# Performance work log

Measured on AMD Instinct MI355X. Metric: run time of the kernel, lower is better.

## Reference

```python
import jax, jax.numpy as jnp
import numpy as np

EPS = 1e-5
GROUPS = 32


def conv2d(x, w, b):
    # x: [N,C,H,W], w: [O,I,3,3] (or 1x1), stride 1, padding 'same' for 3x3
    kh = w.shape[2]
    pad = (kh - 1) // 2
    y = jax.lax.conv_general_dilated(x, w, (1, 1), ((pad, pad), (pad, pad)),
                                     dimension_numbers=('NCHW', 'OIHW', 'NCHW'))
    return y + b[None, :, None, None]


def group_norm(x, g, b):
    N, C, H, W = x.shape
    xr = x.reshape(N, GROUPS, C // GROUPS, H, W)
    mu = xr.mean(axis=(2, 3, 4), keepdims=True)
    var = xr.var(axis=(2, 3, 4), keepdims=True)
    xr = (xr - mu) / jnp.sqrt(var + EPS)
    return xr.reshape(N, C, H, W) * g[None, :, None, None] + b[None, :, None, None]


def batch_norm(x, g, b):
    # training-mode BatchNorm2d: batch statistics over (N,H,W)
    mu = x.mean(axis=(0, 2, 3), keepdims=True)
    var = x.var(axis=(0, 2, 3), keepdims=True)
    return (x - mu) / jnp.sqrt(var + EPS) * g[None, :, None, None] + b[None, :, None, None]


def binary_activation(x):
    # STE: forward sign(x), backward through piecewise poly out3
    out_fwd = jnp.sign(x)
    m1 = (x < -1).astype(x.dtype)
    m2 = (x < 0).astype(x.dtype)
    m3 = (x < 1).astype(x.dtype)
    out1 = -1.0 * m1 + (x * x + 2.0 * x) * (1.0 - m1)
    out2 = out1 * m2 + (-x * x + 2.0 * x) * (1.0 - m2)
    out3 = out2 * m3 + 1.0 * (1.0 - m3)
    return jax.lax.stop_gradient(out_fwd - out3) + out3


def hard_binary_conv(x, w, b):
    # per-output-channel scaling * sign(w), STE through clipped weights
    scale = jax.lax.stop_gradient(jnp.mean(jnp.abs(w), axis=(1, 2, 3), keepdims=True))
    bw_ng = scale * jnp.sign(w)
    clipped = jnp.clip(w, -1.0, 1.0)
    bw = jax.lax.stop_gradient(bw_ng - clipped) + clipped
    return conv2d(x, bw, b)


def learnable_bias(x, emb, w, b):
    bias = jax.nn.silu(emb) @ w.T + b  # [B, C]
    return x + bias[:, :, None, None]


def _forward(c, x, emb,
             rb_gn1_g, rb_gn1_b, rb_conv1_w, rb_conv1_b, rb_emb_w, rb_emb_b,
             rb_gn2_g, rb_gn2_b, rb_conv2_w, rb_conv2_b,
             m1_w, m1_b, bconv_w, bconv_b, bn_g, bn_b,
             m2_w, m2_b, prelu_a, m3_w, m3_b):
    # ResBlock (skip = Identity since out_channels == channels)
    h = conv2d(jax.nn.silu(group_norm(c, rb_gn1_g, rb_gn1_b)), rb_conv1_w, rb_conv1_b)
    eo = jax.nn.silu(emb) @ rb_emb_w.T + rb_emb_b          # [B, 2*C]
    scale, shift = jnp.split(eo[:, :, None, None], 2, axis=1)
    h = group_norm(h, rb_gn2_g, rb_gn2_b) * (1.0 + scale) + shift
    h = conv2d(jax.nn.silu(h), rb_conv2_w, rb_conv2_b)
    c2 = c + h
    # concat + bias + STE binarize + binary conv + BN + channel-pool residual + PReLU
    xc = jnp.concatenate([x, c2], axis=1)                   # [B, 2C, H, W]
    out = learnable_bias(xc, emb, m1_w, m1_b)
    out = binary_activation(out)
    out = hard_binary_conv(out, bconv_w, bconv_b)
    out = batch_norm(out, bn_g, bn_b)
    N, C2, H, W = xc.shape
    out = out + xc.reshape(N, C2 // 2, 2, H, W).mean(axis=2)  # channel mean pooling
    out = learnable_bias(out, emb, m2_w, m2_b)
    out = jnp.where(out >= 0, out, prelu_a[None, :, None, None] * out)  # PReLU
    out = learnable_bias(out, emb, m3_w, m3_b)
    return out


def setup_inputs() -> dict:
    key = jax.random.key(0)
    ks = jax.random.split(key, 24)
    B, C, EMB, H, W = 8, 128, 512, 64, 64
    IN2 = 2 * C
    n = lambda k, s, sc=0.05: jax.random.normal(k, s, dtype=jnp.float32) * sc
    return {
        'c': jax.random.normal(ks[0], (B, C, H, W), dtype=jnp.float32),
        'x': jax.random.normal(ks[1], (B, C, H, W), dtype=jnp.float32),
        'emb': jax.random.normal(ks[2], (B, EMB), dtype=jnp.float32),
        'rb_gn1_g': jnp.ones((C,), jnp.float32), 'rb_gn1_b': jnp.zeros((C,), jnp.float32),
        'rb_conv1_w': n(ks[3], (C, C, 3, 3)), 'rb_conv1_b': n(ks[4], (C,)),
        'rb_emb_w': n(ks[5], (2 * C, EMB)), 'rb_emb_b': n(ks[6], (2 * C,)),
        'rb_gn2_g': jnp.ones((C,), jnp.float32), 'rb_gn2_b': jnp.zeros((C,), jnp.float32),
        'rb_conv2_w': n(ks[7], (C, C, 3, 3)), 'rb_conv2_b': n(ks[8], (C,)),
        'm1_w': n(ks[9], (IN2, EMB)), 'm1_b': n(ks[10], (IN2,)),
        'bconv_w': jax.random.uniform(ks[11], (C, IN2, 3, 3), dtype=jnp.float32) * 0.001,
        'bconv_b': n(ks[12], (C,)),
        'bn_g': jnp.ones((C,), jnp.float32), 'bn_b': jnp.zeros((C,), jnp.float32),
        'm2_w': n(ks[13], (C, EMB)), 'm2_b': n(ks[14], (C,)),
        'prelu_a': jnp.full((C,), 0.25, jnp.float32),
        'm3_w': n(ks[15], (C, EMB)), 'm3_b': n(ks[16], (C,)),
    }


def reference(c, x, emb,
              rb_gn1_g, rb_gn1_b, rb_conv1_w, rb_conv1_b, rb_emb_w, rb_emb_b,
              rb_gn2_g, rb_gn2_b, rb_conv2_w, rb_conv2_b,
              m1_w, m1_b, bconv_w, bconv_b, bn_g, bn_b,
              m2_w, m2_b, prelu_a, m3_w, m3_b):
    return _forward(c, x, emb,
                    rb_gn1_g, rb_gn1_b, rb_conv1_w, rb_conv1_b, rb_emb_w, rb_emb_b,
                    rb_gn2_g, rb_gn2_b, rb_conv2_w, rb_conv2_b,
                    m1_w, m1_b, bconv_w, bconv_b, bn_g, bn_b,
                    m2_w, m2_b, prelu_a, m3_w, m3_b)
```

## Files before the change

kernel.cpp:

```cpp
#include <hip/hip_runtime.h>
#include <stdint.h>


#define B_   8
#define C_   128
#define C2_  256
#define HW_  4096
#define EMB_ 512
#define EPS_ 1e-5f

typedef int   v16i __attribute__((ext_vector_type(16)));
typedef float v16f __attribute__((ext_vector_type(16)));
typedef short v8s  __attribute__((ext_vector_type(8)));
typedef int   v4i  __attribute__((ext_vector_type(4)));

#define COLB 272
#define LDSZ (3 * 66 * COLB)

__device__ __forceinline__ float silu(float v) { return v / (1.f + expf(-v)); }
__device__ __forceinline__ unsigned short f2bf(float f) {
    unsigned int x = __float_as_uint(f);
    return (unsigned short)((x + 0x7FFFu + ((x >> 16) & 1u)) >> 16);
}
__device__ __forceinline__ int8_t sgn8(float v) {
    return (v > 0.f) ? (int8_t)1 : ((v < 0.f) ? (int8_t)(-1) : (int8_t)0);
}

__global__ __launch_bounds__(256) void k_prep(
    const float* __restrict__ w, int8_t* __restrict__ sgn,
    float* __restrict__ alpha, float* __restrict__ bnS, float* __restrict__ bnQ,
    float* __restrict__ gnS, float* __restrict__ gnQ,
    const float* __restrict__ w1, const float* __restrict__ w2,
    unsigned short* __restrict__ Wc1, unsigned short* __restrict__ Wc2,
    const float* __restrict__ emb,
    const float* __restrict__ ew, const float* __restrict__ ebb,
    const float* __restrict__ m1w, const float* __restrict__ m1b,
    const float* __restrict__ m2w, const float* __restrict__ m2b,
    const float* __restrict__ m3w, const float* __restrict__ m3b,
    float* __restrict__ eo, float* __restrict__ b1,
    float* __restrict__ b2, float* __restrict__ b3) {
    __shared__ float red[256];
    const int blk = blockIdx.x, tid = threadIdx.x;
    if (blk < 128) {
        const int o = blk;
        if (o == 0 && tid < 128) { bnS[tid] = 0.f; bnQ[tid] = 0.f; }
        if (o == 1) { gnS[tid] = 0.f; }
        if (o == 2) { gnQ[tid] = 0.f; }
        const float* wr = w + (size_t)o * (C2_ * 9);
        float s = 0.f;
        for (int i = tid; i < C2_ * 9; i += 256) s += fabsf(wr[i]);
        red[tid] = s;
        __syncthreads();
        for (int st = 128; st > 0; st >>= 1) {
            if (tid < st) red[tid] += red[tid + st];
            __syncthreads();
        }
        if (tid == 0) alpha[o] = red[0] / (float)(C2_ * 9);
        for (int kk = 0; kk < 9; ++kk) {
            float v = wr[tid * 9 + kk];
            sgn[((size_t)(kk * 16 + (tid >> 4)) * C_ + o) * 16 + (tid & 15)] = sgn8(v);
        }
    } else if (blk < 704) {
        int i = (blk - 128) * 256 + tid;
        int co = i / (C_ * 9);
        int rem = i - co * (C_ * 9);
        int ci = rem / 9, kk = rem - ci * 9;
        size_t d = ((size_t)(kk * 16 + (ci >> 3)) * C_ + co) * 8 + (ci & 7);
        Wc1[d] = f2bf(w1[i]);
        Wc2[d] = f2bf(w2[i]);
    } else {
        const int o = (blk - 704) * 4 + (tid >> 6);
        const int l = tid & 63;
        const float* wv;
        float bias;
        float* dst;
        int dstride;
        if (o < 256)      { wv = ew  + (size_t)o * EMB_;              bias = ebb[o];    dst = eo + o;  dstride = 256; }
        else if (o < 512) { int r = o - 256; wv = m1w + (size_t)r * EMB_; bias = m1b[r]; dst = b1 + r; dstride = 256; }
        else if (o < 640) { int r = o - 512; wv = m2w + (size_t)r * EMB_; bias = m2b[r]; dst = b2 + r; dstride = 128; }
        else              { int r = o - 640; wv = m3w + (size_t)r * EMB_; bias = m3b[r]; dst = b3 + r; dstride = 128; }
        const float4 wa = *(const float4*)(wv + 8 * l);
        const float4 wb = *(const float4*)(wv + 8 * l + 4);
#pragma unroll
        for (int b = 0; b < B_; ++b) {
            const float* s = emb + b * EMB_ + 8 * l;
            float4 sa = *(const float4*)(s);
            float4 sb = *(const float4*)(s + 4);
            float p = wa.x * silu(sa.x) + wa.y * silu(sa.y) + wa.z * silu(sa.z) + wa.w * silu(sa.w) +
                      wb.x * silu(sb.x) + wb.y * silu(sb.y) + wb.z * silu(sb.z) + wb.w * silu(sb.w);
#pragma unroll
            for (int off = 32; off > 0; off >>= 1) p += __shfl_down(p, off, 64);
            if (l == 0) dst[b * dstride] = bias + p;
        }
    }
}

__global__ __launch_bounds__(1024) void k_gn1t(const float* __restrict__ in,
                                               const float* __restrict__ g,
                                               const float* __restrict__ b,
                                               unsigned short* __restrict__ act) {
    __shared__ float ssum[1024], ssq[1024];
    __shared__ float s_mu, s_rstd;
    const int tid = threadIdx.x;
    const int n = blockIdx.x >> 5, grp = blockIdx.x & 31;
    const size_t base = ((size_t)(n * C_ + grp * 4)) << 12;
    float sum = 0.f, sq = 0.f;
    const float4* in4 = (const float4*)(in + base);
    for (int i = tid; i < 4096; i += 1024) {
        float4 v = in4[i];
        sum += v.x + v.y + v.z + v.w;
        sq += v.x * v.x + v.y * v.y + v.z * v.z + v.w * v.w;
    }
    ssum[tid] = sum; ssq[tid] = sq;
    __syncthreads();
    for (int st = 512; st > 0; st >>= 1) {
        if (tid < st) { ssum[tid] += ssum[tid + st]; ssq[tid] += ssq[tid + st]; }
        __syncthreads();
    }
    if (tid == 0) {
        float mu = ssum[0] * (1.f / 16384.f);
        float var = ssq[0] * (1.f / 16384.f) - mu * mu;
        s_mu = mu; s_rstd = rsqrtf(var + EPS_);
    }
    __syncthreads();
    const float mu = s_mu, rstd = s_rstd;
    float gg[4], bb[4];
#pragma unroll
    for (int j = 0; j < 4; ++j) { gg[j] = g[grp * 4 + j]; bb[j] = b[grp * 4 + j]; }
    for (int hw = tid; hw < HW_; hw += 1024) {
        union { unsigned short u[4]; uint2 v; } pk;
#pragma unroll
        for (int j = 0; j < 4; ++j) {
            float v = in[base + ((size_t)j << 12) + hw];
            pk.u[j] = f2bf(silu((v - mu) * rstd * gg[j] + bb[j]));
        }
        *(uint2*)(act + ((size_t)(n * HW_ + hw)) * C_ + grp * 4) = pk.v;
    }
}

__global__ __launch_bounds__(1024) void k_gn2a(const float* __restrict__ in,
                                               const float* __restrict__ g,
                                               const float* __restrict__ b,
                                               const float* __restrict__ eo,
                                               const float* __restrict__ gnS,
                                               const float* __restrict__ gnQ,
                                               unsigned short* __restrict__ act) {
    const int tid = threadIdx.x;
    const int n = blockIdx.x >> 5, grp = blockIdx.x & 31;
    const size_t base = ((size_t)(n * C_ + grp * 4)) << 12;
    const float mu = gnS[n * 32 + grp] * (1.f / 16384.f);
    const float var = gnQ[n * 32 + grp] * (1.f / 16384.f) - mu * mu;
    const float rstd = rsqrtf(var + EPS_);
    float sc[4], sh[4], gg[4], bb[4];
#pragma unroll
    for (int j = 0; j < 4; ++j) {
        int ch = grp * 4 + j;
        gg[j] = g[ch]; bb[j] = b[ch];
        sc[j] = 1.f + eo[n * 256 + ch];
        sh[j] = eo[n * 256 + 128 + ch];
    }
    for (int hw = tid; hw < HW_; hw += 1024) {
        union { unsigned short u[4]; uint2 v; } pk;
#pragma unroll
        for (int j = 0; j < 4; ++j) {
            float v = in[base + ((size_t)j << 12) + hw];
            float y = ((v - mu) * rstd * gg[j] + bb[j]) * sc[j] + sh[j];
            pk.u[j] = f2bf(silu(y));
        }
        *(uint2*)(act + ((size_t)(n * HW_ + hw)) * C_ + grp * 4) = pk.v;
    }
}

__device__ __forceinline__ void stage_rows(char* lds, const char* rs0,
                                           const char* rs1, const char* rs2) {
    const int tid = threadIdx.x;
    const char* rs[3] = {rs0, rs1, rs2};
    if (tid < 96) {
        int r = tid / 32, q = tid & 31;
        int c = (q >> 4) ? 65 : 0, o = q & 15;
        *(float4*)(lds + (r * 66 + c) * COLB + o * 16) = make_float4(0.f, 0.f, 0.f, 0.f);
    }
#pragma unroll
    for (int u = 0; u < 12; ++u) {
        int idx = u * 256 + tid;
        int r = idx >> 10, rem = idx & 1023;
        int x = rem >> 4, o = rem & 15;
        char* dst = lds + (r * 66 + x + 1) * COLB + o * 16;
        if (rs[r]) *(float4*)dst = *(const float4*)(rs[r] + x * 256 + o * 16);
        else       *(float4*)dst = make_float4(0.f, 0.f, 0.f, 0.f);
    }
}

__global__ __launch_bounds__(256) void k_conv1(const unsigned short* __restrict__ act,
                                               const unsigned short* __restrict__ Wc,
                                               const float* __restrict__ bias,
                                               float* __restrict__ out,
                                               float* __restrict__ gnS,
                                               float* __restrict__ gnQ) {
    __shared__ __align__(16) char lds[LDSZ];
    const int y = blockIdx.x;
    const int n = blockIdx.y;
    const char* base = (const char*)(act + ((size_t)n * 64) * 64 * C_);
    stage_rows(lds,
               (y > 0)  ? base + (size_t)(y - 1) * 16384 : nullptr,
               base + (size_t)y * 16384,
               (y < 63) ? base + (size_t)(y + 1) * 16384 : nullptr);
    __syncthreads();

    const int w = threadIdx.x >> 6;
    const int l = threadIdx.x & 63;
    const int lm = l & 31;
    const int lh = l >> 5;

    v16f acc0, acc1;
#pragma unroll
    for (int i = 0; i < 16; ++i) { acc0[i] = 0.f; acc1[i] = 0.f; }

#pragma unroll
    for (int kk = 0; kk < 9; ++kk) {
        const int r = kk / 3, dx = kk % 3 - 1;
        const char* col0 = lds + (r * 66 + lm + 1 + dx) * COLB + 16 * lh;
        const char* col1 = col0 + 32 * COLB;
        const unsigned short* wbase = Wc + (size_t)(kk * 16 + lh) * C_ * 8 + (32 * w + lm) * 8;
#pragma unroll
        for (int cb = 0; cb < 8; ++cb) {
            v8s a = *(const v8s*)(wbase + (size_t)(2 * cb) * C_ * 8);
            v8s b0 = *(const v8s*)(col0 + 32 * cb);
            v8s b1 = *(const v8s*)(col1 + 32 * cb);
            acc0 = __builtin_amdgcn_mfma_f32_32x32x16_bf16(a, b0, acc0, 0, 0, 0);
            acc1 = __builtin_amdgcn_mfma_f32_32x32x16_bf16(a, b1, acc1, 0, 0, 0);
        }
    }
    float pr[16], qr[16];
#pragma unroll
    for (int r = 0; r < 16; ++r) {
        const int row = (r & 3) + 8 * (r >> 2) + 4 * lh;
        const int co = 32 * w + row;
        const float bv = bias[co];
        const size_t o = (((size_t)n * C_ + co) << 12) + (y << 6);
        float v0 = acc0[r] + bv, v1 = acc1[r] + bv;
        out[o + lm] = v0;
        out[o + 32 + lm] = v1;
        pr[r] = v0 + v1;
        qr[r] = v0 * v0 + v1 * v1;
    }
    __syncthreads();
    float* ldsS = (float*)lds;
    float* ldsQ = (float*)lds + 128;
#pragma unroll
    for (int r = 0; r < 16; ++r) {
        float p = pr[r], q = qr[r];
#pragma unroll
        for (int m = 16; m > 0; m >>= 1) {
            p += __shfl_xor(p, m, 64);
            q += __shfl_xor(q, m, 64);
        }
        if (lm == 0) {
            const int row = (r & 3) + 8 * (r >> 2) + 4 * lh;
            const int co = 32 * w + row;
            ldsS[co] = p;
            ldsQ[co] = q;
        }
    }
    __syncthreads();
    if (threadIdx.x < 32) {
        const int g = threadIdx.x;
        float p = ldsS[4 * g] + ldsS[4 * g + 1] + ldsS[4 * g + 2] + ldsS[4 * g + 3];
        float q = ldsQ[4 * g] + ldsQ[4 * g + 1] + ldsQ[4 * g + 2] + ldsQ[4 * g + 3];
        atomicAdd(&gnS[n * 32 + g], p);
        atomicAdd(&gnQ[n * 32 + g], q);
    }
}

__global__ __launch_bounds__(256) void k_conv2(const unsigned short* __restrict__ act,
                                               const unsigned short* __restrict__ Wc,
                                               const float* __restrict__ bias,
                                               const float* __restrict__ res,
                                               const float* __restrict__ xin,
                                               const float* __restrict__ b1v,
                                               float* __restrict__ out,
                                               int8_t* __restrict__ S) {
    __shared__ __align__(16) char lds[LDSZ];
    const int y = blockIdx.x;
    const int n = blockIdx.y;
    const char* base = (const char*)(act + ((size_t)n * 64) * 64 * C_);
    stage_rows(lds,
               (y > 0)  ? base + (size_t)(y - 1) * 16384 : nullptr,
               base + (size_t)y * 16384,
               (y < 63) ? base + (size_t)(y + 1) * 16384 : nullptr);
    __syncthreads();

    const int w = threadIdx.x >> 6;
    const int l = threadIdx.x & 63;
    const int lm = l & 31;
    const int lh = l >> 5;

    v16f acc0, acc1;
#pragma unroll
    for (int i = 0; i < 16; ++i) { acc0[i] = 0.f; acc1[i] = 0.f; }

#pragma unroll
    for (int kk = 0; kk < 9; ++kk) {
        const int r = kk / 3, dx = kk % 3 - 1;
        const char* col0 = lds + (r * 66 + lm + 1 + dx) * COLB + 16 * lh;
        const char* col1 = col0 + 32 * COLB;
        const unsigned short* wbase = Wc + (size_t)(kk * 16 + lh) * C_ * 8 + (32 * w + lm) * 8;
#pragma unroll
        for (int cb = 0; cb < 8; ++cb) {
            v8s a = *(const v8s*)(wbase + (size_t)(2 * cb) * C_ * 8);
            v8s b0 = *(const v8s*)(col0 + 32 * cb);
            v8s b1 = *(const v8s*)(col1 + 32 * cb);
            acc0 = __builtin_amdgcn_mfma_f32_32x32x16_bf16(a, b0, acc0, 0, 0, 0);
            acc1 = __builtin_amdgcn_mfma_f32_32x32x16_bf16(a, b1, acc1, 0, 0, 0);
        }
    }
    float c2v0[16], c2v1[16];
#pragma unroll
    for (int r = 0; r < 16; ++r) {
        const int row = (r & 3) + 8 * (r >> 2) + 4 * lh;
        const int co = 32 * w + row;
        const float bv = bias[co];
        const size_t o = (((size_t)n * C_ + co) << 12) + (y << 6);
        float v0 = acc0[r] + bv + res[o + lm];
        float v1 = acc1[r] + bv + res[o + 32 + lm];
        out[o + lm] = v0;
        out[o + 32 + lm] = v1;
        c2v0[r] = v0;
        c2v1[r] = v1;
    }

    __syncthreads();
#pragma unroll
    for (int q = 0; q < 4; ++q) {
        const int co0 = 32 * w + 8 * q + 4 * lh;
        const float b0 = b1v[n * 256 + 128 + co0];
        const float b1b = b1v[n * 256 + 128 + co0 + 1];
        const float b2b = b1v[n * 256 + 128 + co0 + 2];
        const float b3b = b1v[n * 256 + 128 + co0 + 3];
        union { int8_t b[4]; int u; } p0, p1;
        p0.b[0] = sgn8(c2v0[4 * q] + b0);  p1.b[0] = sgn8(c2v1[4 * q] + b0);
        p0.b[1] = sgn8(c2v0[4 * q + 1] + b1b); p1.b[1] = sgn8(c2v1[4 * q + 1] + b1b);
        p0.b[2] = sgn8(c2v0[4 * q + 2] + b2b); p1.b[2] = sgn8(c2v1[4 * q + 2] + b2b);
        p0.b[3] = sgn8(c2v0[4 * q + 3] + b3b); p1.b[3] = sgn8(c2v1[4 * q + 3] + b3b);
        *(int*)(lds + lm * COLB + 128 + co0) = p0.u;
        *(int*)(lds + (32 + lm) * COLB + 128 + co0) = p1.u;
    }
#pragma unroll
    for (int u = 0; u < 8; ++u) {
        int idx = u * 256 + threadIdx.x;
        int ch = idx >> 4, seg = idx & 15;
        float4 v = *(const float4*)(xin + (((size_t)(n * C_ + ch)) << 12) + (y << 6) + 4 * seg);
        const float bv = b1v[n * 256 + ch];
        lds[(4 * seg) * COLB + ch]     = sgn8(v.x + bv);
        lds[(4 * seg + 1) * COLB + ch] = sgn8(v.y + bv);
        lds[(4 * seg + 2) * COLB + ch] = sgn8(v.z + bv);
        lds[(4 * seg + 3) * COLB + ch] = sgn8(v.w + bv);
    }
    __syncthreads();
    int8_t* Srow = S + ((size_t)(n * HW_) + (y << 6)) * C2_;
#pragma unroll
    for (int u = 0; u < 4; ++u) {
        int idx = u * 256 + threadIdx.x;
        int px = idx >> 4, c16 = idx & 15;
        *(int4*)(Srow + (size_t)px * C2_ + 16 * c16) = *(const int4*)(lds + px * COLB + 16 * c16);
    }
}

__global__ __launch_bounds__(256) void k_bconv(const int8_t* __restrict__ S,
                                               const int8_t* __restrict__ Wk,
                                               const float* __restrict__ alpha,
                                               const float* __restrict__ bias,
                                               float* __restrict__ out,
                                               float* __restrict__ bnS,
                                               float* __restrict__ bnQ) {
    __shared__ __align__(16) char lds[LDSZ];
    const int y = blockIdx.x;
    const int n = blockIdx.y;
    const char* base = (const char*)(S + ((size_t)n * 64) * 64 * C2_);
    stage_rows(lds,
               (y > 0)  ? base + (size_t)(y - 1) * 16384 : nullptr,
               base + (size_t)y * 16384,
               (y < 63) ? base + (size_t)(y + 1) * 16384 : nullptr);
    __syncthreads();

    const int w = threadIdx.x >> 6;
    const int l = threadIdx.x & 63;
    const int lm = l & 31;
    const int lh = l >> 5;

    v16i acc0, acc1;
#pragma unroll
    for (int i = 0; i < 16; ++i) { acc0[i] = 0; acc1[i] = 0; }

#pragma unroll
    for (int kk = 0; kk < 9; ++kk) {
        const int r = kk / 3, dx = kk % 3 - 1;
        const char* col0 = lds + (r * 66 + lm + 1 + dx) * COLB + 16 * lh;
        const char* col1 = col0 + 32 * COLB;
        const int8_t* wbase = Wk + (size_t)(kk * 16 + lh) * C_ * 16 + (32 * w + lm) * 16;
#pragma unroll
        for (int s = 0; s < 8; ++s) {
            v4i a = *(const v4i*)(wbase + (size_t)(2 * s) * C_ * 16);
            v4i b0 = *(const v4i*)(col0 + 32 * s);
            v4i b1 = *(const v4i*)(col1 + 32 * s);
            acc0 = __builtin_amdgcn_mfma_i32_32x32x32_i8(a, b0, acc0, 0, 0, 0);
            acc1 = __builtin_amdgcn_mfma_i32_32x32x32_i8(a, b1, acc1, 0, 0, 0);
        }
    }

    float pr[16], qr[16];
#pragma unroll
    for (int r = 0; r < 16; ++r) {
        const int row = (r & 3) + 8 * (r >> 2) + 4 * lh;
        const int co = 32 * w + row;
        const float av = alpha[co], bv = bias[co];
        const size_t o = (((size_t)n * C_ + co) << 12) + (y << 6);
        float v0 = av * (float)acc0[r] + bv;
        float v1 = av * (float)acc1[r] + bv;
        out[o + lm]      = v0;
        out[o + 32 + lm] = v1;
        pr[r] = v0 + v1;
        qr[r] = v0 * v0 + v1 * v1;
    }
    __syncthreads();
    float* ldsS = (float*)lds;
    float* ldsQ = (float*)lds + 128;
#pragma unroll
    for (int r = 0; r < 16; ++r) {
        float p = pr[r], q = qr[r];
#pragma unroll
        for (int m = 16; m > 0; m >>= 1) {
            p += __shfl_xor(p, m, 64);
            q += __shfl_xor(q, m, 64);
        }
        if (lm == 0) {
            const int row = (r & 3) + 8 * (r >> 2) + 4 * lh;
            const int co = 32 * w + row;
            ldsS[co] = p;
            ldsQ[co] = q;
        }
    }
    __syncthreads();
    if (threadIdx.x < 128) {
        atomicAdd(&bnS[threadIdx.x], ldsS[threadIdx.x]);
        atomicAdd(&bnQ[threadIdx.x], ldsQ[threadIdx.x]);
    }
}

__global__ __launch_bounds__(256) void k_final(const float* __restrict__ y3,
                                               const float* __restrict__ x,
                                               const float* __restrict__ c2,
                                               const float* __restrict__ bnS,
                                               const float* __restrict__ bnQ,
                                               const float* __restrict__ bng,
                                               const float* __restrict__ bnb,
                                               const float* __restrict__ b2v,
                                               const float* __restrict__ pa,
                                               const float* __restrict__ b3v,
                                               float* __restrict__ out) {
    const int idx4 = blockIdx.x * 256 + threadIdx.x;
    const int hw = (idx4 & 1023) * 4;
    const int cb = idx4 >> 10;
    const int co = cb & 127;
    const int n = cb >> 7;
    const float mu = bnS[co] * (1.f / 32768.f);
    const float var = bnQ[co] * (1.f / 32768.f) - mu * mu;
    const float rstd = rsqrtf(var + EPS_);
    const float gm = rstd * bng[co];
    const float bt = bnb[co] - mu * gm;
    const size_t obase = (((size_t)(n * C_ + co)) << 12) + hw;
    float4 v = *(const float4*)(y3 + obase);
    v.x = v.x * gm + bt; v.y = v.y * gm + bt; v.z = v.z * gm + bt; v.w = v.w * gm + bt;

    const int ch0 = 2 * co;
    float4 pA, pB;
    if (co < 64) {
        pA = *(const float4*)(x + (((size_t)(n * C_ + ch0)) << 12) + hw);
        pB = *(const float4*)(x + (((size_t)(n * C_ + ch0 + 1)) << 12) + hw);
    } else {
        int d = ch0 - 128;
        pA = *(const float4*)(c2 + (((size_t)(n * C_ + d)) << 12) + hw);
        pB = *(const float4*)(c2 + (((size_t)(n * C_ + d + 1)) << 12) + hw);
    }
    const float bias2 = b2v[n * 128 + co];
    const float aP = pa[co];
    const float bias3 = b3v[n * 128 + co];
    float4 r;
    float t;
    t = v.x + 0.5f * (pA.x + pB.x) + bias2; t = (t >= 0.f) ? t : aP * t; r.x = t + bias3;
    t = v.y + 0.5f * (pA.y + pB.y) + bias2; t = (t >= 0.f) ? t : aP * t; r.y = t + bias3;
    t = v.z + 0.5f * (pA.z + pB.z) + bias2; t = (t >= 0.f) ? t : aP * t; r.z = t + bias3;
    t = v.w + 0.5f * (pA.w + pB.w) + bias2; t = (t >= 0.f) ? t : aP * t; r.w = t + bias3;
    *(float4*)(out + obase) = r;
}

extern "C" void kernel_launch(void* const* d_in, const int* in_sizes, int n_in,
                              void* d_out, int out_size, void* d_ws, size_t ws_size,
                              hipStream_t stream) {
    const float* c       = (const float*)d_in[0];
    const float* x       = (const float*)d_in[1];
    const float* emb     = (const float*)d_in[2];
    const float* gn1_g   = (const float*)d_in[3];
    const float* gn1_b   = (const float*)d_in[4];
    const float* conv1_w = (const float*)d_in[5];
    const float* conv1_b = (const float*)d_in[6];
    const float* emb_w   = (const float*)d_in[7];
    const float* emb_b   = (const float*)d_in[8];
    const float* gn2_g   = (const float*)d_in[9];
    const float* gn2_b   = (const float*)d_in[10];
    const float* conv2_w = (const float*)d_in[11];
    const float* conv2_b = (const float*)d_in[12];
    const float* m1_w    = (const float*)d_in[13];
    const float* m1_b    = (const float*)d_in[14];
    const float* bconv_w = (const float*)d_in[15];
    const float* bconv_b = (const float*)d_in[16];
    const float* bn_g    = (const float*)d_in[17];
    const float* bn_b    = (const float*)d_in[18];
    const float* m2_w    = (const float*)d_in[19];
    const float* m2_b    = (const float*)d_in[20];
    const float* prelu_a = (const float*)d_in[21];
    const float* m3_w    = (const float*)d_in[22];
    const float* m3_b    = (const float*)d_in[23];
    float* out = (float*)d_out;

    float* ws = (float*)d_ws;
    const size_t NCHW = (size_t)B_ * C_ * HW_;
    float*  a_buf = ws;
    float*  y_buf = ws + NCHW;
    unsigned short* actA = (unsigned short*)(ws + 2 * NCHW);
    int8_t* S     = (int8_t*)(ws + 2 * NCHW);
    int8_t* sgn   = (int8_t*)(ws + 2 * NCHW + NCHW / 2);
    unsigned short* Wc1 = (unsigned short*)(ws + 2 * NCHW + NCHW / 2 + 73728);
    unsigned short* Wc2 = Wc1 + C_ * C_ * 9;
    float*  alpha = ws + 2 * NCHW + NCHW / 2 + 73728 + 2 * 73728;
    float*  eo    = alpha + 128;
    float*  b1v   = eo + B_ * 256;
    float*  b2v   = b1v + B_ * 256;
    float*  b3v   = b2v + B_ * 128;
    float*  bnS   = b3v + B_ * 128;
    float*  bnQ   = bnS + 128;
    float*  gnS   = bnQ + 128;
    float*  gnQ   = gnS + 256;

    k_prep<<<896, 256, 0, stream>>>(bconv_w, sgn, alpha, bnS, bnQ, gnS, gnQ,
                                    conv1_w, conv2_w, Wc1, Wc2,
                                    emb, emb_w, emb_b, m1_w, m1_b, m2_w, m2_b,
                                    m3_w, m3_b, eo, b1v, b2v, b3v);
    k_gn1t<<<B_ * 32, 1024, 0, stream>>>(c, gn1_g, gn1_b, actA);
    k_conv1<<<dim3(64, B_), 256, 0, stream>>>(actA, Wc1, conv1_b, y_buf, gnS, gnQ);
    k_gn2a<<<B_ * 32, 1024, 0, stream>>>(y_buf, gn2_g, gn2_b, eo, gnS, gnQ, actA);
    k_conv2<<<dim3(64, B_), 256, 0, stream>>>(actA, Wc2, conv2_b, c, x, b1v, a_buf, S);
    k_bconv<<<dim3(64, B_), 256, 0, stream>>>(S, sgn, alpha, bconv_b, y_buf, bnS, bnQ);
    k_final<<<NCHW / 1024, 256, 0, stream>>>(y_buf, x, a_buf, bnS, bnQ, bn_g, bn_b,
                                             b2v, prelu_a, b3v, out);
}
```

Before: 255.4 us.

## Fuse GN1 into prep kernel and GN2 normalization into conv2 staging

The GroupNorm1+SiLU kernel is folded into the prep kernel as extra blocks, which removes one launch and lets it run alongside the weight preparation. The GroupNorm2+modulation+SiLU pass is moved into conv2's LDS staging: conv2 now reads fp32 y1 rows directly, normalizes and converts them to bf16 in shared memory, and no longer needs the intermediate activation buffer. In exchange, each conv2 block recomputes the normalized values for three input rows (a halo redundancy of about 3x). Staging now uses only 192 threads with strided per-channel stores, which may be slower than the previous cooperative copy.

```diff
diff --git a/kernel.cpp b/kernel.cpp
--- a/kernel.cpp
+++ b/kernel.cpp
@@ -38,8 +38,12 @@
     const float* __restrict__ m2w, const float* __restrict__ m2b,
     const float* __restrict__ m3w, const float* __restrict__ m3b,
     float* __restrict__ eo, float* __restrict__ b1,
-    float* __restrict__ b2, float* __restrict__ b3) {
-    __shared__ float red[256];
+    float* __restrict__ b2, float* __restrict__ b3,
+    const float* __restrict__ cin,
+    const float* __restrict__ g1, const float* __restrict__ bb1,
+    unsigned short* __restrict__ act) {
+    __shared__ float red[256], red2[256];
+    __shared__ float s_mu, s_rstd;
     const int blk = blockIdx.x, tid = threadIdx.x;
     if (blk < 128) {
         const int o = blk;
@@ -68,7 +72,7 @@
         size_t d = ((size_t)(kk * 16 + (ci >> 3)) * C_ + co) * 8 + (ci & 7);
         Wc1[d] = f2bf(w1[i]);
         Wc2[d] = f2bf(w2[i]);
-    } else {
+    } else if (blk < 896) {
         const int o = (blk - 704) * 4 + (tid >> 6);
         const int l = tid & 63;
         const float* wv;
@@ -92,82 +96,42 @@
             for (int off = 32; off > 0; off >>= 1) p += __shfl_down(p, off, 64);
             if (l == 0) dst[b * dstride] = bias + p;
         }
-    }
-}
-
-__global__ __launch_bounds__(1024) void k_gn1t(const float* __restrict__ in,
-                                               const float* __restrict__ g,
-                                               const float* __restrict__ b,
-                                               unsigned short* __restrict__ act) {
-    __shared__ float ssum[1024], ssq[1024];
-    __shared__ float s_mu, s_rstd;
-    const int tid = threadIdx.x;
-    const int n = blockIdx.x >> 5, grp = blockIdx.x & 31;
-    const size_t base = ((size_t)(n * C_ + grp * 4)) << 12;
-    float sum = 0.f, sq = 0.f;
-    const float4* in4 = (const float4*)(in + base);
-    for (int i = tid; i < 4096; i += 1024) {
-        float4 v = in4[i];
-        sum += v.x + v.y + v.z + v.w;
-        sq += v.x * v.x + v.y * v.y + v.z * v.z + v.w * v.w;
-    }
-    ssum[tid] = sum; ssq[tid] = sq;
-    __syncthreads();
-    for (int st = 512; st > 0; st >>= 1) {
-        if (tid < st) { ssum[tid] += ssum[tid + st]; ssq[tid] += ssq[tid + st]; }
+    } else {
+        const int bid = blk - 896;
+        const int n = bid >> 5, grp = bid & 31;
+        const size_t base = ((size_t)(n * C_ + grp * 4)) << 12;
+        float sum = 0.f, sq = 0.f;
+        const float4* in4 = (const float4*)(cin + base);
+        for (int i = tid; i < 4096; i += 256) {
+            float4 v = in4[i];
+            sum += v.x + v.y + v.z + v.w;
+            sq += v.x * v.x + v.y * v.y + v.z * v.z + v.w * v.w;
+        }
+        red[tid] = sum; red2[tid] = sq;
         __syncthreads();
-    }
-    if (tid == 0) {
-        float mu = ssum[0] * (1.f / 16384.f);
-        float var = ssq[0] * (1.f / 16384.f) - mu * mu;
-        s_mu = mu; s_rstd = rsqrtf(var + EPS_);
-    }
-    __syncthreads();
-    const float mu = s_mu, rstd = s_rstd;
-    float gg[4], bb[4];
-#pragma unroll
-    for (int j = 0; j < 4; ++j) { gg[j] = g[grp * 4 + j]; bb[j] = b[grp * 4 + j]; }
-    for (int hw = tid; hw < HW_; hw += 1024) {
-        union { unsigned short u[4]; uint2 v; } pk;
-#pragma unroll
-        for (int j = 0; j < 4; ++j) {
-            float v = in[base + ((size_t)j << 12) + hw];
-            pk.u[j] = f2bf(silu((v - mu) * rstd * gg[j] + bb[j]));
-        }
-        *(uint2*)(act + ((size_t)(n * HW_ + hw)) * C_ + grp * 4) = pk.v;
-    }
-}
-
-__global__ __launch_bounds__(1024) void k_gn2a(const float* __restrict__ in,
-                                               const float* __restrict__ g,
-                                               const float* __restrict__ b,
-                                               const float* __restrict__ eo,
-                                               const float* __restrict__ gnS,
-                                               const float* __restrict__ gnQ,
-                                               unsigned short* __restrict__ act) {
-    const int tid = threadIdx.x;
-    const int n = blockIdx.x >> 5, grp = blockIdx.x & 31;
-    const size_t base = ((size_t)(n * C_ + grp * 4)) << 12;
-    const float mu = gnS[n * 32 + grp] * (1.f / 16384.f);
-    const float var = gnQ[n * 32 + grp] * (1.f / 16384.f) - mu * mu;
-    const float rstd = rsqrtf(var + EPS_);
-    float sc[4], sh[4], gg[4], bb[4];
-#pragma unroll
-    for (int j = 0; j < 4; ++j) {
-        int ch = grp * 4 + j;
-        gg[j] = g[ch]; bb[j] = b[ch];
-        sc[j] = 1.f + eo[n * 256 + ch];
-        sh[j] = eo[n * 256 + 128 + ch];
-    }
-    for (int hw = tid; hw < HW_; hw += 1024) {
-        union { unsigned short u[4]; uint2 v; } pk;
-#pragma unroll
-        for (int j = 0; j < 4; ++j) {
-            float v = in[base + ((size_t)j << 12) + hw];
-            float y = ((v - mu) * rstd * gg[j] + bb[j]) * sc[j] + sh[j];
-            pk.u[j] = f2bf(silu(y));
-        }
-        *(uint2*)(act + ((size_t)(n * HW_ + hw)) * C_ + grp * 4) = pk.v;
+        for (int st = 128; st > 0; st >>= 1) {
+            if (tid < st) { red[tid] += red[tid + st]; red2[tid] += red2[tid + st]; }
+            __syncthreads();
+        }
+        if (tid == 0) {
+            float mu = red[0] * (1.f / 16384.f);
+            float var = red2[0] * (1.f / 16384.f) - mu * mu;
+            s_mu = mu; s_rstd = rsqrtf(var + EPS_);
+        }
+        __syncthreads();
+        const float mu = s_mu, rstd = s_rstd;
+        float gg[4], bbv[4];
+#pragma unroll
+        for (int j = 0; j < 4; ++j) { gg[j] = g1[grp * 4 + j]; bbv[j] = bb1[grp * 4 + j]; }
+        for (int hw = tid; hw < HW_; hw += 256) {
+            union { unsigned short u[4]; uint2 v; } pk;
+#pragma unroll
+            for (int j = 0; j < 4; ++j) {
+                float v = cin[base + ((size_t)j << 12) + hw];
+                pk.u[j] = f2bf(silu((v - mu) * rstd * gg[j] + bbv[j]));
+            }
+            *(uint2*)(act + ((size_t)(n * HW_ + hw)) * C_ + grp * 4) = pk.v;
+        }
     }
 }
 
@@ -272,7 +236,12 @@
     }
 }
 
-__global__ __launch_bounds__(256) void k_conv2(const unsigned short* __restrict__ act,
+__global__ __launch_bounds__(256) void k_conv2(const float* __restrict__ y1,
+                                               const float* __restrict__ g2,
+                                               const float* __restrict__ b2g,
+                                               const float* __restrict__ eo,
+                                               const float* __restrict__ gnS,
+                                               const float* __restrict__ gnQ,
                                                const unsigned short* __restrict__ Wc,
                                                const float* __restrict__ bias,
                                                const float* __restrict__ res,
@@ -283,15 +252,58 @@
     __shared__ __align__(16) char lds[LDSZ];
     const int y = blockIdx.x;
     const int n = blockIdx.y;
-    const char* base = (const char*)(act + ((size_t)n * 64) * 64 * C_);
-    stage_rows(lds,
-               (y > 0)  ? base + (size_t)(y - 1) * 16384 : nullptr,
-               base + (size_t)y * 16384,
-               (y < 63) ? base + (size_t)(y + 1) * 16384 : nullptr);
-    __syncthreads();
-
-    const int w = threadIdx.x >> 6;
-    const int l = threadIdx.x & 63;
+    const int tid = threadIdx.x;
+
+    if (tid < 192) {
+        const int r = tid / 64, cp = tid & 63;
+        const int yy = y + r - 1;
+        const int ch0 = 2 * cp;
+        char* dst = lds + (r * 66 + 1) * COLB + 2 * ch0;
+        if (yy < 0 || yy > 63) {
+#pragma unroll
+            for (int x = 0; x < 64; ++x) *(int*)(dst + x * COLB) = 0;
+        } else {
+            const int grp = ch0 >> 2;
+            const float mu = gnS[n * 32 + grp] * (1.f / 16384.f);
+            const float var = gnQ[n * 32 + grp] * (1.f / 16384.f) - mu * mu;
+            const float rstd = rsqrtf(var + EPS_);
+            const float gm0 = rstd * g2[ch0],     bt0 = b2g[ch0] - mu * gm0;
+            const float gm1 = rstd * g2[ch0 + 1], bt1 = b2g[ch0 + 1] - mu * gm1;
+            const float sc0 = 1.f + eo[n * 256 + ch0],     sh0 = eo[n * 256 + 128 + ch0];
+            const float sc1 = 1.f + eo[n * 256 + ch0 + 1], sh1 = eo[n * 256 + 128 + ch0 + 1];
+            const float* p0 = y1 + (((size_t)(n * C_ + ch0)) << 12) + (yy << 6);
+            const float* p1 = p0 + HW_;
+#pragma unroll
+            for (int xq = 0; xq < 16; ++xq) {
+                float4 v0 = *(const float4*)(p0 + 4 * xq);
+                float4 v1 = *(const float4*)(p1 + 4 * xq);
+                float a0, a1;
+                a0 = silu((v0.x * gm0 + bt0) * sc0 + sh0);
+                a1 = silu((v1.x * gm1 + bt1) * sc1 + sh1);
+                *(int*)(dst + (4 * xq) * COLB) = ((int)f2bf(a1) << 16) | (int)f2bf(a0);
+                a0 = silu((v0.y * gm0 + bt0) * sc0 + sh0);
+                a1 = silu((v1.y * gm1 + bt1) * sc1 + sh1);
+                *(int*)(dst + (4 * xq + 1) * COLB) = ((int)f2bf(a1) << 16) | (int)f2bf(a0);
+                a0 = silu((v0.z * gm0 + bt0) * sc0 + sh0);
+                a1 = silu((v1.z * gm1 + bt1) * sc1 + sh1);
+                *(int*)(dst + (4 * xq + 2) * COLB) = ((int)f2bf(a1) << 16) | (int)f2bf(a0);
+                a0 = silu((v0.w * gm0 + bt0) * sc0 + sh0);
+                a1 = silu((v1.w * gm1 + bt1) * sc1 + sh1);
+                *(int*)(dst + (4 * xq + 3) * COLB) = ((int)f2bf(a1) << 16) | (int)f2bf(a0);
+            }
+        }
+    } else {
+        const int t2 = tid - 192;
+#pragma unroll
+        for (int p = 0; p < 6; ++p) {
+            int r = p >> 1, col = (p & 1) ? 65 : 0;
+            *(int*)(lds + (r * 66 + col) * COLB + 4 * t2) = 0;
+        }
+    }
+    __syncthreads();
+
+    const int w = tid >> 6;
+    const int l = tid & 63;
     const int lm = l & 31;
     const int lh = l >> 5;
 
@@ -338,7 +350,7 @@
         const float b2b = b1v[n * 256 + 128 + co0 + 2];
         const float b3b = b1v[n * 256 + 128 + co0 + 3];
         union { int8_t b[4]; int u; } p0, p1;
-        p0.b[0] = sgn8(c2v0[4 * q] + b0);  p1.b[0] = sgn8(c2v1[4 * q] + b0);
+        p0.b[0] = sgn8(c2v0[4 * q] + b0);      p1.b[0] = sgn8(c2v1[4 * q] + b0);
         p0.b[1] = sgn8(c2v0[4 * q + 1] + b1b); p1.b[1] = sgn8(c2v1[4 * q + 1] + b1b);
         p0.b[2] = sgn8(c2v0[4 * q + 2] + b2b); p1.b[2] = sgn8(c2v1[4 * q + 2] + b2b);
         p0.b[3] = sgn8(c2v0[4 * q + 3] + b3b); p1.b[3] = sgn8(c2v1[4 * q + 3] + b3b);
@@ -347,7 +359,7 @@
     }
 #pragma unroll
     for (int u = 0; u < 8; ++u) {
-        int idx = u * 256 + threadIdx.x;
+        int idx = u * 256 + tid;
         int ch = idx >> 4, seg = idx & 15;
         float4 v = *(const float4*)(xin + (((size_t)(n * C_ + ch)) << 12) + (y << 6) + 4 * seg);
         const float bv = b1v[n * 256 + ch];
@@ -360,7 +372,7 @@
     int8_t* Srow = S + ((size_t)(n * HW_) + (y << 6)) * C2_;
 #pragma unroll
     for (int u = 0; u < 4; ++u) {
-        int idx = u * 256 + threadIdx.x;
+        int idx = u * 256 + tid;
         int px = idx >> 4, c16 = idx & 15;
         *(int4*)(Srow + (size_t)px * C2_ + 16 * c16) = *(const int4*)(lds + px * COLB + 16 * c16);
     }
@@ -542,14 +554,14 @@
     float*  gnS   = bnQ + 128;
     float*  gnQ   = gnS + 256;
 
-    k_prep<<<896, 256, 0, stream>>>(bconv_w, sgn, alpha, bnS, bnQ, gnS, gnQ,
-                                    conv1_w, conv2_w, Wc1, Wc2,
-                                    emb, emb_w, emb_b, m1_w, m1_b, m2_w, m2_b,
-                                    m3_w, m3_b, eo, b1v, b2v, b3v);
-    k_gn1t<<<B_ * 32, 1024, 0, stream>>>(c, gn1_g, gn1_b, actA);
+    k_prep<<<1152, 256, 0, stream>>>(bconv_w, sgn, alpha, bnS, bnQ, gnS, gnQ,
+                                     conv1_w, conv2_w, Wc1, Wc2,
+                                     emb, emb_w, emb_b, m1_w, m1_b, m2_w, m2_b,
+                                     m3_w, m3_b, eo, b1v, b2v, b3v,
+                                     c, gn1_g, gn1_b, actA);
     k_conv1<<<dim3(64, B_), 256, 0, stream>>>(actA, Wc1, conv1_b, y_buf, gnS, gnQ);
-    k_gn2a<<<B_ * 32, 1024, 0, stream>>>(y_buf, gn2_g, gn2_b, eo, gnS, gnQ, actA);
-    k_conv2<<<dim3(64, B_), 256, 0, stream>>>(actA, Wc2, conv2_b, c, x, b1v, a_buf, S);
+    k_conv2<<<dim3(64, B_), 256, 0, stream>>>(y_buf, gn2_g, gn2_b, eo, gnS, gnQ,
+                                              Wc2, conv2_b, c, x, b1v, a_buf, S);
     k_bconv<<<dim3(64, B_), 256, 0, stream>>>(S, sgn, alpha, bconv_b, y_buf, bnS, bnQ);
     k_final<<<NCHW / 1024, 256, 0, stream>>>(y_buf, x, a_buf, bnS, bnQ, bn_g, bn_b,
                                              b2v, prelu_a, b3v, out);
```

New measurement: 260.6 us. +2.0%, slower.
